# Performance work log

Hardware: AMD Instinct MI355X
Metric: run time of the kernel (lower is better)

## Reference

```python
import jax, jax.numpy as jnp
import numpy as np

N, NF, DIM, H, DH, DEPTH, EDIM, NB = 256, 127, 128, 8, 64, 6, 3, 512
INNER = H * DH  # 512
SCALE = DH ** -0.5
EPS = 1e-5


def setup_inputs() -> dict:
    key = jax.random.key(0)
    ks = jax.random.split(key, 16)
    p = lambda k, shape: jax.random.normal(k, shape, jnp.float32) * 0.02
    return {
        "coordinates": jax.random.normal(ks[0], (N, 3), jnp.float32),
        "bonds": jax.random.randint(ks[1], (NB, 2), 0, N),
        "noise_level": jax.random.uniform(ks[2], (1,), jnp.float32),
        "atom_emb": p(ks[3], (N, NF)),
        "ln1_g": jnp.ones((DEPTH, DIM)), "ln1_b": jnp.zeros((DEPTH, DIM)),
        "Wq": p(ks[4], (DEPTH, DIM, INNER)), "bq": jnp.zeros((DEPTH, INNER)),
        "Wkv": p(ks[5], (DEPTH, DIM, 2 * INNER)), "bkv": jnp.zeros((DEPTH, 2 * INNER)),
        "We": p(ks[6], (DEPTH, EDIM, INNER)), "be": jnp.zeros((DEPTH, INNER)),
        "Wo": p(ks[7], (DEPTH, INNER, DIM)), "bo": jnp.zeros((DEPTH, DIM)),
        "Wg1": p(ks[8], (DEPTH, 3 * DIM)),
        "ln2_g": jnp.ones((DEPTH, DIM)), "ln2_b": jnp.zeros((DEPTH, DIM)),
        "W1": p(ks[9], (DEPTH, DIM, 4 * DIM)), "b1": jnp.zeros((DEPTH, 4 * DIM)),
        "W2": p(ks[10], (DEPTH, 4 * DIM, DIM)), "b2": jnp.zeros((DEPTH, DIM)),
        "Wg2": p(ks[11], (DEPTH, 3 * DIM)),
        "out_w": p(ks[12], (DIM, 1)), "out_b": jnp.zeros((1,)),
    }


def _layernorm(x, g, b):
    m = jnp.mean(x, axis=-1, keepdims=True)
    v = jnp.mean((x - m) ** 2, axis=-1, keepdims=True)
    return (x - m) * jax.lax.rsqrt(v + EPS) * g + b


def _gated_residual(x, res, Wg):
    # Linear(3*dim -> 1, no bias) then sigmoid; mask is all-True so no masking.
    gate = jax.nn.sigmoid(jnp.concatenate([x, res, x - res], axis=-1) @ Wg)[..., None]
    return x * gate + res * (1.0 - gate)


def _forward(coordinates, bonds, noise_level, atom_emb, ln1_g, ln1_b, Wq, bq,
             Wkv, bkv, We, be, Wo, bo, Wg1, ln2_g, ln2_b, W1, b1, W2, b2, Wg2,
             out_w, out_b):
    n = coordinates.shape[0]
    # nodes: [n, NF] atom embeddings (looked up at arange(n)) + noise column -> [n, DIM]
    noise_col = jnp.broadcast_to(noise_level.reshape(1, 1), (n, 1))
    nodes = jnp.concatenate([atom_emb, noise_col], axis=-1)
    # dense edge tensor [n, n, 3]: coordinate differences at bonded pairs, antisymmetric
    bi, bj = bonds[:, 0], bonds[:, 1]
    diff = coordinates[bi] - coordinates[bj]
    edges = jnp.zeros((n, n, EDIM), jnp.float32).at[bi, bj].set(diff).at[bj, bi].set(-diff)

    for l in range(DEPTH):
        # --- edge-biased multi-head attention (PreNorm) ---
        x = _layernorm(nodes, ln1_g[l], ln1_b[l])
        q = (x @ Wq[l] + bq[l]).reshape(n, H, DH).transpose(1, 0, 2)          # [h, i, d]
        kv = x @ Wkv[l] + bkv[l]
        k = kv[:, :INNER].reshape(n, H, DH).transpose(1, 0, 2)                # [h, j, d]
        v = kv[:, INNER:].reshape(n, H, DH).transpose(1, 0, 2)                # [h, j, d]
        e = (edges @ We[l] + be[l]).reshape(n, n, H, DH).transpose(2, 0, 1, 3)  # [h, i, j, d]
        k_ij = k[:, None, :, :] + e                                            # [h, i, j, d]
        v_ij = v[:, None, :, :] + e
        sim = jnp.einsum('hid,hijd->hij', q, k_ij) * SCALE
        attn = jax.nn.softmax(sim, axis=-1)  # mask is all ones -> no-op
        out = jnp.einsum('hij,hijd->hid', attn, v_ij)                          # [h, i, d]
        out = out.transpose(1, 0, 2).reshape(n, INNER) @ Wo[l] + bo[l]         # [n, DIM]
        nodes = _gated_residual(out, nodes, Wg1[l])
        # --- feedforward (PreNorm) + gated residual ---
        y = _layernorm(nodes, ln2_g[l], ln2_b[l])
        y = jax.nn.gelu(y @ W1[l] + b1[l], approximate=False) @ W2[l] + b2[l]
        nodes = _gated_residual(y, nodes, Wg2[l])

    energy = nodes @ out_w + out_b  # [n, 1]
    return energy[None, :, :]       # [1, n, 1]


def reference(coordinates, bonds, noise_level, atom_emb, ln1_g, ln1_b, Wq, bq,
              Wkv, bkv, We, be, Wo, bo, Wg1, ln2_g, ln2_b, W1, b1, W2, b2, Wg2,
              out_w, out_b):
    return _forward(coordinates, bonds, noise_level, atom_emb, ln1_g, ln1_b,
                    Wq, bq, Wkv, bkv, We, be, Wo, bo, Wg1, ln2_g, ln2_b,
                    W1, b1, W2, b2, Wg2, out_w, out_b)
```

## Files before the change

### kernel.cpp

```cpp
#include <hip/hip_runtime.h>

#define NN     256
#define NF     127
#define DIM    128
#define NH     8
#define DH     64
#define INNER  512
#define DEPTH  6
#define NB     512
#define ATTN_SCALE 0.125f
#define LN_EPS 1e-5f

#define FMA4(A_, S_, V_) { A_.x=fmaf(S_,(V_).x,A_.x); A_.y=fmaf(S_,(V_).y,A_.y); \
                           A_.z=fmaf(S_,(V_).z,A_.z); A_.w=fmaf(S_,(V_).w,A_.w); }

__device__ __forceinline__ float wred_sum(float v){
#pragma unroll
  for(int o=32;o;o>>=1) v += __shfl_xor(v,o);
  return v;
}
__device__ __forceinline__ float wred_max(float v){
#pragma unroll
  for(int o=32;o;o>>=1) v = fmaxf(v,__shfl_xor(v,o));
  return v;
}
__device__ __forceinline__ float2 wred_sum2(float a, float b){
#pragma unroll
  for(int o=32;o;o>>=1){ a += __shfl_xor(a,o); b += __shfl_xor(b,o); }
  return make_float2(a,b);
}

__device__ __forceinline__ void ln_wave(float n0, float n1,
                                        const float* g, const float* b, int l,
                                        float& x0, float& x1){
  float2 sv = wred_sum2(n0+n1, n0*n0+n1*n1);
  float m  = sv.x*(1.f/DIM);
  float var = sv.y*(1.f/DIM) - m*m;
  float rs = rsqrtf(var + LN_EPS);
  x0 = (n0-m)*rs*g[l]    + b[l];
  x1 = (n1-m)*rs*g[64+l] + b[64+l];
}

__device__ __forceinline__ void gate_wave(float o0, float o1, float& n0, float& n1,
                                          const float* Wg, int l){
  float gv = o0*Wg[l]    + n0*Wg[DIM+l]    + (o0-n0)*Wg[2*DIM+l]
           + o1*Wg[64+l] + n1*Wg[DIM+64+l] + (o1-n1)*Wg[2*DIM+64+l];
  gv = wred_sum(gv);
  float gate = 1.f/(1.f + expf(-gv));
  n0 = o0*gate + n0*(1.f-gate);
  n1 = o1*gate + n1*(1.f-gate);
}

__device__ __forceinline__ void mvp128_512(const float* __restrict__ xin,
                                           const float* __restrict__ W,
                                           float* __restrict__ SC, int t){
  const int cg4 = (t&127)<<2, f0 = (t>>7)<<5;
  const float* __restrict__ p = W + f0*INNER + cg4;
  float4 a0 = make_float4(0.f,0.f,0.f,0.f), a1 = a0;
#pragma unroll
  for(int k=0;k<16;k++){
    float4 w0 = *(const float4*)(p + k*INNER);
    float4 w1 = *(const float4*)(p + (16+k)*INNER);
    float x0 = xin[f0+k], x1 = xin[f0+16+k];
    FMA4(a0, x0, w0); FMA4(a1, x1, w1);
  }
  a0.x+=a1.x; a0.y+=a1.y; a0.z+=a1.z; a0.w+=a1.w;
  *(float4*)(SC + (t>>7)*INNER + cg4) = a0;
}
__device__ __forceinline__ void mvp128_1024(const float* __restrict__ xin,
                                            const float* __restrict__ W,
                                            float* __restrict__ SC, int t){
  const int cg4 = (t&255)<<2, f0 = (t>>8)<<6;
  const float* __restrict__ p = W + f0*(2*INNER) + cg4;
  float4 a0 = make_float4(0.f,0.f,0.f,0.f), a1 = a0;
#pragma unroll
  for(int k=0;k<32;k++){
    float4 w0 = *(const float4*)(p + k*(2*INNER));
    float4 w1 = *(const float4*)(p + (32+k)*(2*INNER));
    float x0 = xin[f0+k], x1 = xin[f0+32+k];
    FMA4(a0, x0, w0); FMA4(a1, x1, w1);
  }
  a0.x+=a1.x; a0.y+=a1.y; a0.z+=a1.z; a0.w+=a1.w;
  *(float4*)(SC + (t>>8)*(2*INNER) + cg4) = a0;
}
__device__ __forceinline__ void mvp512_128(const float* __restrict__ ain,
                                           const float* __restrict__ W,
                                           float* __restrict__ SC, int t){
  const int cg4 = (t&31)<<2, f0 = (t>>5)<<5;
  const float* __restrict__ p = W + f0*DIM + cg4;
  float4 a0 = make_float4(0.f,0.f,0.f,0.f), a1 = a0;
#pragma unroll
  for(int k=0;k<16;k++){
    float4 w0 = *(const float4*)(p + k*DIM);
    float4 w1 = *(const float4*)(p + (16+k)*DIM);
    float x0 = ain[f0+k], x1 = ain[f0+16+k];
    FMA4(a0, x0, w0); FMA4(a1, x1, w1);
  }
  a0.x+=a1.x; a0.y+=a1.y; a0.z+=a1.z; a0.w+=a1.w;
  *(float4*)(SC + (t>>5)*DIM + cg4) = a0;
}

__device__ __forceinline__ void qkv_tail(const float* __restrict__ xs, int i,
    const float* __restrict__ Wq, const float* __restrict__ bq,
    const float* __restrict__ Wkv, const float* __restrict__ bkv,
    const float* __restrict__ be, float* qgn, float* kTn, float* vgn,
    float* __restrict__ SC, int t){
  mvp128_512 (xs, Wq,  SC,        t);
  mvp128_1024(xs, Wkv, SC + 2048, t);
  __syncthreads();
  qgn[i*INNER + t] = bq[t] + SC[t] + SC[INNER+t] + SC[2*INNER+t] + SC[3*INNER+t];
#pragma unroll
  for(int cc=0; cc<2; cc++){
    int c = t + cc*512;
    float s = bkv[c] + SC[2048 + c] + SC[2048 + 1024 + c];
    if(c < INNER) kTn[c*NN + i]            = s + be[c];
    else          vgn[i*INNER + c - INNER] = s + be[c-INNER];
  }
}

__global__ __launch_bounds__(512) void k_qkv0(const float* atom_emb, const float* noise,
    float* nodes, const float* ln1_g, const float* ln1_b,
    const float* Wq, const float* bq, const float* Wkv, const float* bkv, const float* be,
    float* qg, float* kT, float* vg){
  __shared__ __align__(16) float SC[4096];
  __shared__ __align__(16) float xsm[DIM];
  const int t = threadIdx.x, i = blockIdx.x;
  const int w = t>>6, l = t&63;
  float nd0 = (l<NF)?    atom_emb[i*NF + l]      : noise[0];
  float nd1 = (64+l<NF)? atom_emb[i*NF + 64 + l] : noise[0];
  if(w==0){ nodes[i*DIM + l] = nd0; nodes[i*DIM + 64 + l] = nd1; }
  float x0, x1;
  ln_wave(nd0, nd1, ln1_g, ln1_b, l, x0, x1);
  xsm[l] = x0; xsm[64+l] = x1;
  __syncthreads();
  qkv_tail(xsm, i, Wq, bq, Wkv, bkv, be, qg, kT, vg, SC, t);
}

__global__ __launch_bounds__(512) void k_attn(
    const float* __restrict__ qg, const float* __restrict__ kT,
    const float* __restrict__ vg,
    const int* __restrict__ bonds, const float* __restrict__ coords,
    const float* __restrict__ We, float* __restrict__ aog)
{
  __shared__ __align__(16) float qsm[8*DH];
  __shared__ __align__(16) float eb[8][3*NN];
  __shared__ __align__(16) float aW[8][NN];
  const int t = threadIdx.x;
  const int h = blockIdx.x >> 5, i0 = (blockIdx.x & 31) << 3;
  const int w = t>>6, l = t&63;
  const int qb = h*DH, j0 = l<<2;

  qsm[w*DH + l] = qg[(i0+w)*INNER + qb + l];
#pragma unroll
  for(int cc=0; cc<12; cc++) (&eb[0][0])[cc*512 + t] = 0.f;
  __syncthreads();

  {
    const int bi = bonds[2*t], bj = bonds[2*t+1];
    const bool hi = (bi>=i0 && bi<i0+8), hj = (bj>=i0 && bj<i0+8);
    if(hi || hj){
      float dx = coords[3*bi+0] - coords[3*bj+0];
      float dy = coords[3*bi+1] - coords[3*bj+1];
      float dz = coords[3*bi+2] - coords[3*bj+2];
      if(hi){ float* e = eb[bi-i0]; e[bj]=dx;  e[NN+bj]=dy;  e[2*NN+bj]=dz;  }
      if(hj){ float* e = eb[bj-i0]; e[bi]=-dx; e[NN+bi]=-dy; e[2*NN+bi]=-dz; }
    }
  }
  __syncthreads();

  float qwe0, qwe1, qwe2;
  {
    float qv = qsm[w*DH + l];
    qwe0 = qv*We[0*INNER + qb + l];
    qwe1 = qv*We[1*INNER + qb + l];
    qwe2 = qv*We[2*INNER + qb + l];
#pragma unroll
    for(int o=32;o;o>>=1){
      qwe0 += __shfl_xor(qwe0,o); qwe1 += __shfl_xor(qwe1,o); qwe2 += __shfl_xor(qwe2,o);
    }
  }
  const float* __restrict__ kTh = kT + qb*NN + j0;
  float s0=0.f,s1=0.f,s2=0.f,s3=0.f;
  float u0=0.f,u1=0.f,u2=0.f,u3=0.f;
#pragma unroll
  for(int o=0;o<32;o++){
    float4 ka = *(const float4*)(kTh + o*NN);
    float4 kb = *(const float4*)(kTh + (32+o)*NN);
    float qa = qsm[w*DH + o], qc = qsm[w*DH + 32 + o];
    s0=fmaf(qa,ka.x,s0); s1=fmaf(qa,ka.y,s1); s2=fmaf(qa,ka.z,s2); s3=fmaf(qa,ka.w,s3);
    u0=fmaf(qc,kb.x,u0); u1=fmaf(qc,kb.y,u1); u2=fmaf(qc,kb.z,u2); u3=fmaf(qc,kb.w,u3);
  }
  s0+=u0; s1+=u1; s2+=u2; s3+=u3;
  const float* e = eb[w];
  float4 ex = *(const float4*)(e + j0);
  float4 ey = *(const float4*)(e + NN + j0);
  float4 ez = *(const float4*)(e + 2*NN + j0);
  s0 = (s0 + qwe0*ex.x + qwe1*ey.x + qwe2*ez.x)*ATTN_SCALE;
  s1 = (s1 + qwe0*ex.y + qwe1*ey.y + qwe2*ez.y)*ATTN_SCALE;
  s2 = (s2 + qwe0*ex.z + qwe1*ey.z + qwe2*ez.z)*ATTN_SCALE;
  s3 = (s3 + qwe0*ex.w + qwe1*ey.w + qwe2*ez.w)*ATTN_SCALE;
  float mx = wred_max(fmaxf(fmaxf(s0,s1),fmaxf(s2,s3)));
  float p0=expf(s0-mx), p1=expf(s1-mx), p2=expf(s2-mx), p3=expf(s3-mx);
  float inv = 1.f / wred_sum(p0+p1+p2+p3);
  float a0=p0*inv, a1=p1*inv, a2=p2*inv, a3=p3*inv;
  *(float4*)(aW[w] + j0) = make_float4(a0,a1,a2,a3);
  float c0 = a0*ex.x + a1*ex.y + a2*ex.z + a3*ex.w;
  float c1 = a0*ey.x + a1*ey.y + a2*ey.z + a3*ey.w;
  float c2 = a0*ez.x + a1*ez.y + a2*ez.z + a3*ez.w;
  c0 = wred_sum(c0); c1 = wred_sum(c1); c2 = wred_sum(c2);
  __builtin_amdgcn_wave_barrier();
  const int dq = (l&15)<<2, jg = l>>4;
  const float* __restrict__ vb = vg + qb + dq;
  const float* aWw = aW[w];
  float4 acc = make_float4(0.f,0.f,0.f,0.f), acc2 = acc;
#pragma unroll
  for(int jj=0;jj<32;jj++){
    int ja = (jg<<6) + jj, jb = ja + 32;
    float4 va = *(const float4*)(vb + ja*INNER);
    float4 vv = *(const float4*)(vb + jb*INNER);
    FMA4(acc,  aWw[ja], va);
    FMA4(acc2, aWw[jb], vv);
  }
  acc.x+=acc2.x; acc.y+=acc2.y; acc.z+=acc2.z; acc.w+=acc2.w;
#pragma unroll
  for(int o=16;o<64;o<<=1){
    acc.x += __shfl_xor(acc.x,o); acc.y += __shfl_xor(acc.y,o);
    acc.z += __shfl_xor(acc.z,o); acc.w += __shfl_xor(acc.w,o);
  }
  if(l<16){
    float4 we0 = *(const float4*)(We + 0*INNER + qb + dq);
    float4 we1 = *(const float4*)(We + 1*INNER + qb + dq);
    float4 we2 = *(const float4*)(We + 2*INNER + qb + dq);
    float4 ov;
    ov.x = acc.x + c0*we0.x + c1*we1.x + c2*we2.x;
    ov.y = acc.y + c0*we0.y + c1*we1.y + c2*we2.y;
    ov.z = acc.z + c0*we0.z + c1*we1.z + c2*we2.z;
    ov.w = acc.w + c0*we0.w + c1*we1.w + c2*we2.w;
    *(float4*)(aog + (i0+w)*INNER + qb + dq) = ov;
  }
}

__global__ __launch_bounds__(512) void k_layer(
    float* nodes, const float* __restrict__ aog,
    float* qg_n, float* kT_n, float* vg_n,
    const float* __restrict__ Wo, const float* __restrict__ bo,
    const float* __restrict__ Wg1,
    const float* __restrict__ ln2_g, const float* __restrict__ ln2_b,
    const float* __restrict__ W1, const float* __restrict__ b1,
    const float* __restrict__ W2, const float* __restrict__ b2,
    const float* __restrict__ Wg2,
    const float* __restrict__ ln1_g_n, const float* __restrict__ ln1_b_n,
    const float* __restrict__ Wq_n, const float* __restrict__ bq_n,
    const float* __restrict__ Wkv_n, const float* __restrict__ bkv_n,
    const float* __restrict__ be_n,
    const float* __restrict__ out_w, const float* __restrict__ out_b,
    float* eout, int has_next)
{
  __shared__ __align__(16) float SC[4096];
  __shared__ __align__(16) float qs[INNER];
  __shared__ __align__(16) float aos[INNER];
  __shared__ __align__(16) float xsm[DIM];
  const int t = threadIdx.x, i = blockIdx.x;
  const int w = t>>6, l = t&63;

  aos[t] = aog[i*INNER + t];
  float nd0 = nodes[i*DIM + l];
  float nd1 = nodes[i*DIM + 64 + l];
  __syncthreads();

  mvp512_128(aos, Wo, SC, t);
  __syncthreads();
  {
    float o0 = bo[l], o1 = bo[64+l];
#pragma unroll
    for(int fg=0; fg<16; fg++){ o0 += SC[fg*DIM + l]; o1 += SC[fg*DIM + 64 + l]; }
    gate_wave(o0, o1, nd0, nd1, Wg1, l);
    float x0, x1;
    ln_wave(nd0, nd1, ln2_g, ln2_b, l, x0, x1);
    xsm[l] = x0; xsm[64+l] = x1;
  }
  __syncthreads();

  mvp128_512(xsm, W1, SC, t);
  __syncthreads();
  {
    float a = b1[t] + SC[t] + SC[INNER+t] + SC[2*INNER+t] + SC[3*INNER+t];
    qs[t] = 0.5f*a*(1.f + erff(a*0.70710678118654752440f));
  }
  __syncthreads();
  mvp512_128(qs, W2, SC, t);
  __syncthreads();
  {
    float y0 = b2[l], y1 = b2[64+l];
#pragma unroll
    for(int fg=0; fg<16; fg++){ y0 += SC[fg*DIM + l]; y1 += SC[fg*DIM + 64 + l]; }
    gate_wave(y0, y1, nd0, nd1, Wg2, l);
    if(w==0){ nodes[i*DIM + l] = nd0; nodes[i*DIM + 64 + l] = nd1; }
    if(has_next){
      float x0, x1;
      ln_wave(nd0, nd1, ln1_g_n, ln1_b_n, l, x0, x1);
      xsm[l] = x0; xsm[64+l] = x1;
    } else if(w==0){
      float ev = nd0*out_w[l] + nd1*out_w[64+l];
      ev = wred_sum(ev);
      if(l==0) eout[i] = ev + out_b[0];
    }
  }
  if(has_next){
    __syncthreads();
    qkv_tail(xsm, i, Wq_n, bq_n, Wkv_n, bkv_n, be_n,
             qg_n, kT_n, vg_n, SC, t);
  }
}

extern "C" void kernel_launch(void* const* d_in, const int* in_sizes, int n_in,
                              void* d_out, int out_size, void* d_ws, size_t ws_size,
                              hipStream_t stream){
  const float* coords   = (const float*)d_in[0];
  const int*   bonds    = (const int*  )d_in[1];
  const float* noise    = (const float*)d_in[2];
  const float* atom_emb = (const float*)d_in[3];
  const float* ln1_g = (const float*)d_in[4];
  const float* ln1_b = (const float*)d_in[5];
  const float* Wq    = (const float*)d_in[6];
  const float* bq    = (const float*)d_in[7];
  const float* Wkv   = (const float*)d_in[8];
  const float* bkv   = (const float*)d_in[9];
  const float* We    = (const float*)d_in[10];
  const float* be    = (const float*)d_in[11];
  const float* Wo    = (const float*)d_in[12];
  const float* bo    = (const float*)d_in[13];
  const float* Wg1   = (const float*)d_in[14];
  const float* ln2_g = (const float*)d_in[15];
  const float* ln2_b = (const float*)d_in[16];
  const float* W1    = (const float*)d_in[17];
  const float* b1    = (const float*)d_in[18];
  const float* W2    = (const float*)d_in[19];
  const float* b2    = (const float*)d_in[20];
  const float* Wg2   = (const float*)d_in[21];
  const float* out_w = (const float*)d_in[22];
  const float* out_b = (const float*)d_in[23];

  float* ws = (float*)d_ws;
  float* nodes   = ws;
  float* qbuf[2] = { ws +  32768, ws + 163840 };
  float* kbuf[2] = { ws + 294912, ws + 425984 };
  float* vbuf[2] = { ws + 557056, ws + 688128 };
  float* aobuf   = ws + 819200;

  k_qkv0<<<NN, 512, 0, stream>>>(atom_emb, noise, nodes, ln1_g, ln1_b,
                                 Wq, bq, Wkv, bkv, be,
                                 qbuf[0], kbuf[0], vbuf[0]);
  for(int l=0; l<DEPTH; l++){
    int cur = l&1, nxt = cur^1;
    int has_next = (l < DEPTH-1);
    int ln = has_next ? l+1 : l;
    k_attn<<<NN, 512, 0, stream>>>(
      qbuf[cur], kbuf[cur], vbuf[cur], bonds, coords,
      We + (size_t)l*3*INNER, aobuf);
    k_layer<<<NN, 512, 0, stream>>>(
      nodes, aobuf,
      qbuf[nxt], kbuf[nxt], vbuf[nxt],
      Wo  + (size_t)l*INNER*DIM, bo + (size_t)l*DIM, Wg1 + (size_t)l*3*DIM,
      ln2_g + (size_t)l*DIM, ln2_b + (size_t)l*DIM,
      W1  + (size_t)l*DIM*4*DIM, b1 + (size_t)l*4*DIM,
      W2  + (size_t)l*4*DIM*DIM, b2 + (size_t)l*DIM, Wg2 + (size_t)l*3*DIM,
      ln1_g + (size_t)ln*DIM, ln1_b + (size_t)ln*DIM,
      Wq  + (size_t)ln*DIM*INNER, bq + (size_t)ln*INNER,
      Wkv + (size_t)ln*DIM*2*INNER, bkv + (size_t)ln*2*INNER,
      be  + (size_t)ln*INNER,
      out_w, out_b, (float*)d_out, has_next);
  }
}
```

Measured before the change: 312.1 us.

## Stage weight matrices through LDS with double-buffered async global-to-LDS loads

Replaces the per-thread direct global float4 loads in the three matrix-vector helpers with one templated routine. It streams each weight matrix in 32 KB chunks into a double-buffered LDS staging area using the global_load_lds builtin, then has threads read their columns from LDS. The goal is to overlap fetching the next chunk with compute on the current one and to coalesce the weight traffic. In exchange it needs a block-wide barrier per chunk, keeps only one chunk in flight, uses a single accumulator per thread, and raises LDS use to about 72 KB per block. Q and KV projections now run one after the other instead of sharing one scratch pass.

```diff
diff --git a/kernel.cpp b/kernel.cpp
--- a/kernel.cpp
+++ b/kernel.cpp
@@ -11,6 +11,8 @@
 #define ATTN_SCALE 0.125f
 #define LN_EPS 1e-5f
 
+typedef unsigned int u32;
+
 #define FMA4(A_, S_, V_) { A_.x=fmaf(S_,(V_).x,A_.x); A_.y=fmaf(S_,(V_).y,A_.y); \
                            A_.z=fmaf(S_,(V_).z,A_.z); A_.w=fmaf(S_,(V_).w,A_.w); }
 
@@ -51,70 +53,64 @@
   n1 = o1*gate + n1*(1.f-gate);
 }
 
-__device__ __forceinline__ void mvp128_512(const float* __restrict__ xin,
-                                           const float* __restrict__ W,
-                                           float* __restrict__ SC, int t){
-  const int cg4 = (t&127)<<2, f0 = (t>>7)<<5;
-  const float* __restrict__ p = W + f0*INNER + cg4;
-  float4 a0 = make_float4(0.f,0.f,0.f,0.f), a1 = a0;
-#pragma unroll
-  for(int k=0;k<16;k++){
-    float4 w0 = *(const float4*)(p + k*INNER);
-    float4 w1 = *(const float4*)(p + (16+k)*INNER);
-    float x0 = xin[f0+k], x1 = xin[f0+16+k];
-    FMA4(a0, x0, w0); FMA4(a1, x1, w1);
-  }
-  a0.x+=a1.x; a0.y+=a1.y; a0.z+=a1.z; a0.w+=a1.w;
-  *(float4*)(SC + (t>>7)*INNER + cg4) = a0;
-}
-__device__ __forceinline__ void mvp128_1024(const float* __restrict__ xin,
-                                            const float* __restrict__ W,
-                                            float* __restrict__ SC, int t){
-  const int cg4 = (t&255)<<2, f0 = (t>>8)<<6;
-  const float* __restrict__ p = W + f0*(2*INNER) + cg4;
-  float4 a0 = make_float4(0.f,0.f,0.f,0.f), a1 = a0;
-#pragma unroll
-  for(int k=0;k<32;k++){
-    float4 w0 = *(const float4*)(p + k*(2*INNER));
-    float4 w1 = *(const float4*)(p + (32+k)*(2*INNER));
-    float x0 = xin[f0+k], x1 = xin[f0+32+k];
-    FMA4(a0, x0, w0); FMA4(a1, x1, w1);
-  }
-  a0.x+=a1.x; a0.y+=a1.y; a0.z+=a1.z; a0.w+=a1.w;
-  *(float4*)(SC + (t>>8)*(2*INNER) + cg4) = a0;
-}
-__device__ __forceinline__ void mvp512_128(const float* __restrict__ ain,
-                                           const float* __restrict__ W,
-                                           float* __restrict__ SC, int t){
-  const int cg4 = (t&31)<<2, f0 = (t>>5)<<5;
-  const float* __restrict__ p = W + f0*DIM + cg4;
-  float4 a0 = make_float4(0.f,0.f,0.f,0.f), a1 = a0;
-#pragma unroll
-  for(int k=0;k<16;k++){
-    float4 w0 = *(const float4*)(p + k*DIM);
-    float4 w1 = *(const float4*)(p + (16+k)*DIM);
-    float x0 = ain[f0+k], x1 = ain[f0+16+k];
-    FMA4(a0, x0, w0); FMA4(a1, x1, w1);
-  }
-  a0.x+=a1.x; a0.y+=a1.y; a0.z+=a1.z; a0.w+=a1.w;
-  *(float4*)(SC + (t>>5)*DIM + cg4) = a0;
+__device__ __forceinline__ void gld16(const float* g, float* l){
+  __builtin_amdgcn_global_load_lds(
+      (const __attribute__((address_space(1))) u32*)g,
+      (__attribute__((address_space(3))) u32*)l,
+      16, 0, 0);
+}
+__device__ __forceinline__ void stage32k(const float* __restrict__ g,
+                                         float* stg, int t){
+  const int w = t>>6, l = t&63;
+#pragma unroll
+  for(int r=0;r<4;r++){
+    const int q = (r<<3) + w;
+    gld16(g + q*256 + (l<<2), stg + q*256);
+  }
+}
+
+template<int NCOLS, int NCHUNK>
+__device__ __forceinline__ void mv_staged(const float* __restrict__ xin,
+                                          const float* __restrict__ W,
+                                          float* __restrict__ stg,
+                                          float* __restrict__ SC, int t){
+  constexpr int GROUPS = NCOLS/4;
+  constexpr int RPC    = 8192/NCOLS;
+  const int cg = (t & (GROUPS-1))<<2;
+  const int s  = t / GROUPS;
+  const int r0 = s<<2;
+  float4 acc = make_float4(0.f,0.f,0.f,0.f);
+  stage32k(W, stg, t);
+#pragma unroll
+  for(int c=0; c<NCHUNK; c++){
+    __syncthreads();
+    if(c+1<NCHUNK) stage32k(W + (size_t)(c+1)*8192, stg + ((c+1)&1)*8192, t);
+    const float* ch = stg + (c&1)*8192;
+#pragma unroll
+    for(int k=0;k<4;k++){
+      float x = xin[c*RPC + r0 + k];
+      float4 wv = *(const float4*)(ch + (r0+k)*NCOLS + cg);
+      FMA4(acc, x, wv);
+    }
+  }
+  *(float4*)(SC + s*NCOLS + cg) = acc;
+  __syncthreads();
 }
 
 __device__ __forceinline__ void qkv_tail(const float* __restrict__ xs, int i,
     const float* __restrict__ Wq, const float* __restrict__ bq,
     const float* __restrict__ Wkv, const float* __restrict__ bkv,
     const float* __restrict__ be, float* qgn, float* kTn, float* vgn,
-    float* __restrict__ SC, int t){
-  mvp128_512 (xs, Wq,  SC,        t);
-  mvp128_1024(xs, Wkv, SC + 2048, t);
-  __syncthreads();
+    float* __restrict__ stg, float* __restrict__ SC, int t){
+  mv_staged<512,8>(xs, Wq, stg, SC, t);
   qgn[i*INNER + t] = bq[t] + SC[t] + SC[INNER+t] + SC[2*INNER+t] + SC[3*INNER+t];
+  mv_staged<1024,16>(xs, Wkv, stg, SC, t);
 #pragma unroll
   for(int cc=0; cc<2; cc++){
     int c = t + cc*512;
-    float s = bkv[c] + SC[2048 + c] + SC[2048 + 1024 + c];
-    if(c < INNER) kTn[c*NN + i]            = s + be[c];
-    else          vgn[i*INNER + c - INNER] = s + be[c-INNER];
+    float sv = bkv[c] + SC[c] + SC[1024 + c];
+    if(c < INNER) kTn[c*NN + i]            = sv + be[c];
+    else          vgn[i*INNER + c - INNER] = sv + be[c-INNER];
   }
 }
 
@@ -122,7 +118,8 @@
     float* nodes, const float* ln1_g, const float* ln1_b,
     const float* Wq, const float* bq, const float* Wkv, const float* bkv, const float* be,
     float* qg, float* kT, float* vg){
-  __shared__ __align__(16) float SC[4096];
+  __shared__ __align__(16) float stg[16384];
+  __shared__ __align__(16) float SC[2048];
   __shared__ __align__(16) float xsm[DIM];
   const int t = threadIdx.x, i = blockIdx.x;
   const int w = t>>6, l = t&63;
@@ -133,7 +130,7 @@
   ln_wave(nd0, nd1, ln1_g, ln1_b, l, x0, x1);
   xsm[l] = x0; xsm[64+l] = x1;
   __syncthreads();
-  qkv_tail(xsm, i, Wq, bq, Wkv, bkv, be, qg, kT, vg, SC, t);
+  qkv_tail(xsm, i, Wq, bq, Wkv, bkv, be, qg, kT, vg, stg, SC, t);
 }
 
 __global__ __launch_bounds__(512) void k_attn(
@@ -256,7 +253,8 @@
     const float* __restrict__ out_w, const float* __restrict__ out_b,
     float* eout, int has_next)
 {
-  __shared__ __align__(16) float SC[4096];
+  __shared__ __align__(16) float stg[16384];
+  __shared__ __align__(16) float SC[2048];
   __shared__ __align__(16) float qs[INNER];
   __shared__ __align__(16) float aos[INNER];
   __shared__ __align__(16) float xsm[DIM];
@@ -268,8 +266,7 @@
   float nd1 = nodes[i*DIM + 64 + l];
   __syncthreads();
 
-  mvp512_128(aos, Wo, SC, t);
-  __syncthreads();
+  mv_staged<128,8>(aos, Wo, stg, SC, t);
   {
     float o0 = bo[l], o1 = bo[64+l];
 #pragma unroll
@@ -279,17 +276,13 @@
     ln_wave(nd0, nd1, ln2_g, ln2_b, l, x0, x1);
     xsm[l] = x0; xsm[64+l] = x1;
   }
-  __syncthreads();
-
-  mvp128_512(xsm, W1, SC, t);
-  __syncthreads();
+
+  mv_staged<512,8>(xsm, W1, stg, SC, t);
   {
     float a = b1[t] + SC[t] + SC[INNER+t] + SC[2*INNER+t] + SC[3*INNER+t];
     qs[t] = 0.5f*a*(1.f + erff(a*0.70710678118654752440f));
   }
-  __syncthreads();
-  mvp512_128(qs, W2, SC, t);
-  __syncthreads();
+  mv_staged<128,8>(qs, W2, stg, SC, t);
   {
     float y0 = b2[l], y1 = b2[64+l];
 #pragma unroll
@@ -307,9 +300,8 @@
     }
   }
   if(has_next){
-    __syncthreads();
     qkv_tail(xsm, i, Wq_n, bq_n, Wkv_n, bkv_n, be_n,
-             qg_n, kT_n, vg_n, SC, t);
+             qg_n, kT_n, vg_n, stg, SC, t);
   }
 }
 
```

Result: slower. 384.4 us (+23.2%).
